# Performance work log

Measured on AMD Instinct MI355X. Metric: run time of the kernel, lower is better.

## Reference

```python
import jax, jax.numpy as jnp
import numpy as np

B, S, C, M, L = 32, 8192, 64, 16, 4  # batch, seq, n_enc, n_modes, n_layers


def setup_inputs() -> dict:
    key = jax.random.key(0)
    ks = jax.random.split(key, 12)
    scale = 1.0 / (C * M)
    return {
        "input_tensor": jax.random.normal(ks[0], (B, S, 1), dtype=jnp.float32),
        "enc_w": jax.random.normal(ks[1], (C, 1), dtype=jnp.float32) * 0.1,
        "enc_b": jax.random.normal(ks[2], (C,), dtype=jnp.float32) * 0.1,
        "R_re": jax.random.normal(ks[3], (L, C, C, M), dtype=jnp.float32) * scale,
        "R_im": jax.random.normal(ks[4], (L, C, C, M), dtype=jnp.float32) * scale,
        "Wl_w": jax.random.normal(ks[5], (L, C, C), dtype=jnp.float32) * 0.1,
        "Wl_b": jax.random.normal(ks[6], (L, C), dtype=jnp.float32) * 0.1,
        "d1_w": jax.random.normal(ks[7], (C, C), dtype=jnp.float32) * 0.1,
        "d1_b": jax.random.normal(ks[8], (C,), dtype=jnp.float32) * 0.1,
        "d2_w": jax.random.normal(ks[9], (1, C), dtype=jnp.float32) * 0.1,
        "d2_b": jax.random.normal(ks[10], (1,), dtype=jnp.float32) * 0.1,
    }


def reference(input_tensor, enc_w, enc_b, R_re, R_im, Wl_w, Wl_b, d1_w, d1_b, d2_w, d2_b):
    # encoder: Conv1d(1, C, k=1) == per-position dense over channel dim
    h = jnp.einsum('bsi,ci->bsc', input_tensor, enc_w) + enc_b  # [B,S,C]
    n_freq = S // 2 + 1
    for l in range(L):
        x_cs = jnp.swapaxes(h, 1, 2)                 # [B,C,S]
        x_ft = jnp.fft.rfft(x_cs, axis=-1)           # [B,C,n_freq] complex
        Rl = R_re[l] + 1j * R_im[l]                  # [C,C,M]
        y = jnp.einsum('bim,iom->bom', x_ft[:, :, :M], Rl)  # [B,C,M]
        y_full = jnp.concatenate(
            [y, jnp.zeros((B, C, n_freq - M), dtype=y.dtype)], axis=-1)
        spat = jnp.fft.irfft(y_full, n=S, axis=-1)   # [B,C,S] float32
        wout = jnp.einsum('oi,bis->bos', Wl_w[l], x_cs) + Wl_b[l][None, :, None]
        h = jax.nn.gelu(jnp.swapaxes(spat + wout, 1, 2), approximate=False)
    z = jax.nn.gelu(jnp.einsum('bsc,oc->bso', h, d1_w) + d1_b, approximate=False)
    out = jnp.einsum('bso,po->bsp', z, d2_w) + d2_b  # [B,S,1]
    return out
```

## Files before the change

kernel.cpp:

```cpp
#include <hip/hip_runtime.h>
#include <math.h>

#define NB 32
#define NS 8192
#define NC 64
#define NM 16
#define NL 4
#define NM2 32
#define NSBF 32
#define TPOS 128
#define PAD 65

typedef float f16v __attribute__((ext_vector_type(16)));

static __device__ __forceinline__ f16v zero16() {
    f16v v;
    #pragma unroll
    for (int j = 0; j < 16; ++j) v[j] = 0.0f;
    return v;
}

static __device__ __forceinline__ float gelu_exact(float v) {
    return 0.5f * v * (1.0f + erff(v * 0.7071067811865475f));
}

__global__ void k_table(float* __restrict__ T) {
    int s = blockIdx.x * blockDim.x + threadIdx.x;
    if (s >= NS) return;
    const float w = 6.283185307179586f / (float)NS;
    float* row = T + (size_t)s * NM2;
    #pragma unroll
    for (int m = 0; m < NM; ++m) {
        int idx = (m * s) & (NS - 1);
        float a = w * (float)idx;
        float sv, cv;
        sincosf(a, &sv, &cv);
        row[2*m]   = cv;
        row[2*m+1] = sv;
    }
}

__global__ void k_prep(const float* __restrict__ Ww, const float* __restrict__ d1w,
                       float* __restrict__ Wt, float* __restrict__ d1t) {
    int idx = blockIdx.x * 256 + threadIdx.x;
    if (idx < NL*NC*NC) {
        int l = idx / (NC*NC), r = idx % (NC*NC);
        int i = r / NC, o = r % NC;
        Wt[idx] = Ww[(size_t)l*NC*NC + (size_t)o*NC + i];
    } else if (idx < NL*NC*NC + NC*NC) {
        int r = idx - NL*NC*NC;
        int i = r / NC, o = r % NC;
        d1t[r] = d1w[(size_t)o*NC + i];
    }
}

__global__ void __launch_bounds__(256) k_enc(const float* __restrict__ x,
                                             const float* __restrict__ ew,
                                             const float* __restrict__ eb,
                                             float* __restrict__ h) {
    int t = threadIdx.x;
    int base = blockIdx.x * 64;
    float4* hout = (float4*)(h + (size_t)base * NC);
    #pragma unroll
    for (int j = 0; j < 4; ++j) {
        int idx = t + 256*j;
        int sl = idx >> 4, q = idx & 15;
        float xv = x[base + sl];
        float4 w4 = ((const float4*)ew)[q];
        float4 b4 = ((const float4*)eb)[q];
        hout[idx] = make_float4(fmaf(xv, w4.x, b4.x), fmaf(xv, w4.y, b4.y),
                                fmaf(xv, w4.z, b4.z), fmaf(xv, w4.w, b4.w));
    }
}

__global__ void __launch_bounds__(256) k_fwd(const float* __restrict__ h,
                                             const float* __restrict__ T,
                                             float* __restrict__ partial) {
    __shared__ float red[4 * NC * 33];
    int b = blockIdx.y, sb = blockIdx.x;
    int t = threadIdx.x;
    int w = t >> 6, lane = t & 63;
    const int PPW = NS / NSBF / 4;
    f16v A0 = zero16(), A1 = zero16();
    int s0 = sb * (NS / NSBF) + w * PPW;
    const float* hp = h + ((size_t)b*NS + s0)*NC + lane;
    #pragma unroll 2
    for (int it = 0; it < PPW; ++it) {
        float hv = hp[(size_t)it * NC];
        int su = __builtin_amdgcn_readfirstlane(s0 + it);
        const f16v* tr = (const f16v*)(T + (size_t)su * NM2);
        A0 += hv * tr[0];
        A1 += hv * tr[1];
    }
    float* rr = &red[(w*NC + lane) * 33];
    #pragma unroll
    for (int j = 0; j < 16; ++j) rr[j] = A0[j];
    #pragma unroll
    for (int j = 0; j < 16; ++j) rr[16 + j] = A1[j];
    __syncthreads();
    float* pout = partial + ((size_t)b*NSBF + sb) * (NC*NM2);
    #pragma unroll
    for (int e = 0; e < (NC*NM2)/256; ++e) {
        int idx = t + 256*e;
        int c = idx >> 5, k = idx & 31;
        pout[idx] = red[c*33 + k] + red[(NC + c)*33 + k]
                  + red[(2*NC + c)*33 + k] + red[(3*NC + c)*33 + k];
    }
}

__global__ void __launch_bounds__(256) k_mix(const float* __restrict__ partial,
                                             const float* __restrict__ Rre,
                                             const float* __restrict__ Rim,
                                             float* __restrict__ yst, int l) {
    __shared__ float xf[NC*NM2];
    int b = blockIdx.x, jg = blockIdx.y, t = threadIdx.x;
    #pragma unroll
    for (int e = 0; e < (NC*NM2)/256; ++e) {
        int idx = t + 256*e;
        float s = 0.f;
        #pragma unroll 8
        for (int sb = 0; sb < NSBF; ++sb)
            s += partial[((size_t)b*NSBF + sb)*(NC*NM2) + idx];
        xf[idx] = s;
    }
    __syncthreads();
    {
        int p = t + 256*jg;
        int o = p >> 4, m = p & 15;
        float yre = 0.f, yim = 0.f;
        #pragma unroll 8
        for (int i = 0; i < NC; ++i) {
            float xr = xf[i*NM2 + 2*m];
            float xs = xf[i*NM2 + 2*m + 1];
            size_t ridx = (((size_t)l*NC + i)*NC + o)*NM + m;
            float rr = Rre[ridx], ri = Rim[ridx];
            yre = fmaf(xr, rr, yre); yre = fmaf(xs, ri, yre);
            yim = fmaf(xr, ri, yim); yim = fmaf(-xs, rr, yim);
        }
        float* yb = yst + (size_t)b*NM2*NC;
        if (m == 0) { yb[o] = yre * (1.0f/NS); yb[NC + o] = 0.f; }
        else {
            yb[(size_t)(2*m)*NC + o]   = yre * (2.0f/NS);
            yb[(size_t)(2*m+1)*NC + o] = -yim * (2.0f/NS);
        }
    }
}

__global__ void __launch_bounds__(256) k_spec(float* __restrict__ h,
                                              const float* __restrict__ yst,
                                              const float* __restrict__ Wt,
                                              const float* __restrict__ Wb,
                                              int l) {
    __shared__ float hs[TPOS * PAD];
    int b = blockIdx.y;
    int t = threadIdx.x;
    int og = __builtin_amdgcn_readfirstlane(t >> 6);
    int p  = t & 63;
    int s0 = blockIdx.x * TPOS;

    const float4* hblk = (const float4*)(h + ((size_t)b*NS + s0)*NC);
    float4 ld0 = hblk[t];
    float4 ld1 = hblk[t + 256];
    float4 ld2 = hblk[t + 512];
    float4 ld3 = hblk[t + 768];
    float4 ld4 = hblk[t + 1024];
    float4 ld5 = hblk[t + 1280];
    float4 ld6 = hblk[t + 1536];
    float4 ld7 = hblk[t + 1792];

    const float* Wl = Wt + (size_t)l*NC*NC + og*16;
    const float* bl = Wb + (size_t)l*NC + og*16;
    const float* yb = yst + (size_t)b*NM2*NC + og*16;

    f16v accA = *(const f16v*)bl;
    f16v accB = accA;

    {
        f16v y0 = *(const f16v*)yb;
        accA += y0;
        accB += y0;
        const float w1 = 6.283185307179586f / (float)NS;
        float angA = (float)(s0 + p) * w1;
        float angB = (float)(s0 + p + 64) * w1;
        float cA1, sA1, cB1, sB1;
        sincosf(angA, &sA1, &cA1);
        sincosf(angB, &sB1, &cB1);
        float cmA = cA1, smA = sA1, cmB = cB1, smB = sB1;
        #pragma unroll 1
        for (int m = 1; m < NM; ++m) {
            f16v yc  = *(const f16v*)(yb + (size_t)(2*m)*NC);
            f16v ysv = *(const f16v*)(yb + (size_t)(2*m+1)*NC);
            accA += cmA * yc;  accA += smA * ysv;
            accB += cmB * yc;  accB += smB * ysv;
            float cnA = cmA*cA1 - smA*sA1;
            smA = cmA*sA1 + smA*cA1;  cmA = cnA;
            float cnB = cmB*cB1 - smB*sB1;
            smB = cmB*sB1 + smB*cB1;  cmB = cnB;
        }
    }

    {
        int ss = t >> 4, q4 = (t & 15) * 4;
        float* d;
        d = &hs[ss*PAD + q4];        d[0]=ld0.x; d[1]=ld0.y; d[2]=ld0.z; d[3]=ld0.w;
        d = &hs[(ss+16)*PAD + q4];   d[0]=ld1.x; d[1]=ld1.y; d[2]=ld1.z; d[3]=ld1.w;
        d = &hs[(ss+32)*PAD + q4];   d[0]=ld2.x; d[1]=ld2.y; d[2]=ld2.z; d[3]=ld2.w;
        d = &hs[(ss+48)*PAD + q4];   d[0]=ld3.x; d[1]=ld3.y; d[2]=ld3.z; d[3]=ld3.w;
        d = &hs[(ss+64)*PAD + q4];   d[0]=ld4.x; d[1]=ld4.y; d[2]=ld4.z; d[3]=ld4.w;
        d = &hs[(ss+80)*PAD + q4];   d[0]=ld5.x; d[1]=ld5.y; d[2]=ld5.z; d[3]=ld5.w;
        d = &hs[(ss+96)*PAD + q4];   d[0]=ld6.x; d[1]=ld6.y; d[2]=ld6.z; d[3]=ld6.w;
        d = &hs[(ss+112)*PAD + q4];  d[0]=ld7.x; d[1]=ld7.y; d[2]=ld7.z; d[3]=ld7.w;
    }
    __syncthreads();

    const float* hA = &hs[p * PAD];
    const float* hB = &hs[(p + 64) * PAD];
    #pragma unroll 8
    for (int i = 0; i < NC; ++i) {
        float va = hA[i], vb = hB[i];
        f16v w = *(const f16v*)(Wl + (size_t)i*NC);
        accA += va * w;
        accB += vb * w;
    }

    float* hpA = h + ((size_t)b*NS + s0 + p)*NC + og*16;
    float* hpB = h + ((size_t)b*NS + s0 + p + 64)*NC + og*16;
    f16v g;
    #pragma unroll
    for (int j = 0; j < 16; ++j) g[j] = gelu_exact(accA[j]);
    *(f16v*)hpA = g;
    #pragma unroll
    for (int j = 0; j < 16; ++j) g[j] = gelu_exact(accB[j]);
    *(f16v*)hpB = g;
}

__global__ void __launch_bounds__(256) k_dec(const float* __restrict__ h,
                                             const float* __restrict__ d1t,
                                             const float* __restrict__ d1b,
                                             const float* __restrict__ d2w,
                                             const float* __restrict__ d2b,
                                             float* __restrict__ out) {
    __shared__ float hs[TPOS * PAD];
    __shared__ float red[4 * TPOS];
    int t = threadIdx.x;
    int og = __builtin_amdgcn_readfirstlane(t >> 6);
    int p  = t & 63;
    int p0 = blockIdx.x * TPOS;

    const float4* hblk = (const float4*)(h + (size_t)p0 * NC);
    float4 ld0 = hblk[t];
    float4 ld1 = hblk[t + 256];
    float4 ld2 = hblk[t + 512];
    float4 ld3 = hblk[t + 768];
    float4 ld4 = hblk[t + 1024];
    float4 ld5 = hblk[t + 1280];
    float4 ld6 = hblk[t + 1536];
    float4 ld7 = hblk[t + 1792];
    {
        int ss = t >> 4, q4 = (t & 15) * 4;
        float* d;
        d = &hs[ss*PAD + q4];        d[0]=ld0.x; d[1]=ld0.y; d[2]=ld0.z; d[3]=ld0.w;
        d = &hs[(ss+16)*PAD + q4];   d[0]=ld1.x; d[1]=ld1.y; d[2]=ld1.z; d[3]=ld1.w;
        d = &hs[(ss+32)*PAD + q4];   d[0]=ld2.x; d[1]=ld2.y; d[2]=ld2.z; d[3]=ld2.w;
        d = &hs[(ss+48)*PAD + q4];   d[0]=ld3.x; d[1]=ld3.y; d[2]=ld3.z; d[3]=ld3.w;
        d = &hs[(ss+64)*PAD + q4];   d[0]=ld4.x; d[1]=ld4.y; d[2]=ld4.z; d[3]=ld4.w;
        d = &hs[(ss+80)*PAD + q4];   d[0]=ld5.x; d[1]=ld5.y; d[2]=ld5.z; d[3]=ld5.w;
        d = &hs[(ss+96)*PAD + q4];   d[0]=ld6.x; d[1]=ld6.y; d[2]=ld6.z; d[3]=ld6.w;
        d = &hs[(ss+112)*PAD + q4];  d[0]=ld7.x; d[1]=ld7.y; d[2]=ld7.z; d[3]=ld7.w;
    }
    __syncthreads();

    f16v accA = *(const f16v*)(d1b + og*16);
    f16v accB = accA;
    const float* hA = &hs[p * PAD];
    const float* hB = &hs[(p + 64) * PAD];
    #pragma unroll 8
    for (int i = 0; i < NC; ++i) {
        float va = hA[i], vb = hB[i];
        f16v w = *(const f16v*)(d1t + (size_t)i*NC + og*16);
        accA += va * w;
        accB += vb * w;
    }
    float resA = 0.f, resB = 0.f;
    #pragma unroll
    for (int j = 0; j < 16; ++j) {
        float dw = d2w[og*16 + j];
        resA = fmaf(gelu_exact(accA[j]), dw, resA);
        resB = fmaf(gelu_exact(accB[j]), dw, resB);
    }
    red[og*TPOS + p]      = resA;
    red[og*TPOS + p + 64] = resB;
    __syncthreads();
    if (t < TPOS) {
        out[p0 + t] = d2b[0] + red[t] + red[TPOS + t]
                    + red[2*TPOS + t] + red[3*TPOS + t];
    }
}

extern "C" void kernel_launch(void* const* d_in, const int* in_sizes, int n_in,
                              void* d_out, int out_size, void* d_ws, size_t ws_size,
                              hipStream_t stream) {
    const float* input = (const float*)d_in[0];
    const float* enc_w = (const float*)d_in[1];
    const float* enc_b = (const float*)d_in[2];
    const float* R_re  = (const float*)d_in[3];
    const float* R_im  = (const float*)d_in[4];
    const float* Wl_w  = (const float*)d_in[5];
    const float* Wl_b  = (const float*)d_in[6];
    const float* d1_w  = (const float*)d_in[7];
    const float* d1_b  = (const float*)d_in[8];
    const float* d2_w  = (const float*)d_in[9];
    const float* d2_b  = (const float*)d_in[10];
    float* out = (float*)d_out;

    float* ws  = (float*)d_ws;
    float* h   = ws;
    float* T   = h   + (size_t)NB*NS*NC;
    float* par = T   + (size_t)NS*NM2;
    float* yst = par + (size_t)NB*NSBF*NC*NM2;
    float* Wt  = yst + (size_t)NB*NM2*NC;
    float* d1t = Wt  + (size_t)NL*NC*NC;

    hipLaunchKernelGGL(k_table, dim3(NS/256), dim3(256), 0, stream, T);
    hipLaunchKernelGGL(k_prep, dim3((NL*NC*NC + NC*NC + 255)/256), dim3(256), 0,
                       stream, Wl_w, d1_w, Wt, d1t);
    hipLaunchKernelGGL(k_enc, dim3((NB*NS)/64), dim3(256), 0, stream,
                       input, enc_w, enc_b, h);
    for (int l = 0; l < NL; ++l) {
        hipLaunchKernelGGL(k_fwd, dim3(NSBF, NB), dim3(256), 0, stream, h, T, par);
        hipLaunchKernelGGL(k_mix, dim3(NB, 4), dim3(256), 0, stream,
                           par, R_re, R_im, yst, l);
        hipLaunchKernelGGL(k_spec, dim3(NS/TPOS, NB), dim3(256), 0, stream,
                           h, yst, Wt, Wl_b, l);
    }
    hipLaunchKernelGGL(k_dec, dim3((NB*NS)/TPOS), dim3(256), 0, stream,
                       h, d1t, d1_b, d2_w, d2_b, out);
}
```

Measured before the change: 402.7 us.

## Fuse forward DFT projection into encoder and spectral layer kernels, fold decoder into last layer

Moves the truncated-DFT projection onto the first 16 modes into the epilogue of the encoder and spectral-layer kernels. It works on the tile already in shared memory, so the separate k_fwd pass that re-read h from global memory is gone. The last layer computes the decoder MLP in place and never writes h back, which removes the k_dec kernel and one full read and write of h. The cost is more partial sums (64 tiles per batch instead of 32) for k_mix to reduce, extra shared-memory syncs, and more register pressure in the spectral kernel.

```diff
diff --git a/kernel.cpp b/kernel.cpp
--- a/kernel.cpp
+++ b/kernel.cpp
@@ -7,16 +7,17 @@
 #define NM 16
 #define NL 4
 #define NM2 32
-#define NSBF 32
 #define TPOS 128
+#define NT (NS/TPOS)
 #define PAD 65
 
 typedef float f16v __attribute__((ext_vector_type(16)));
-
-static __device__ __forceinline__ f16v zero16() {
-    f16v v;
-    #pragma unroll
-    for (int j = 0; j < 16; ++j) v[j] = 0.0f;
+typedef float f8v  __attribute__((ext_vector_type(8)));
+
+static __device__ __forceinline__ f8v zero8() {
+    f8v v;
+    #pragma unroll
+    for (int j = 0; j < 8; ++j) v[j] = 0.0f;
     return v;
 }
 
@@ -54,84 +55,81 @@
     }
 }
 
+static __device__ __forceinline__ void dft_phase(
+        const float* __restrict__ hs, const float* __restrict__ T,
+        float* __restrict__ partial, int b, int tile, int s0,
+        int og, int t) {
+    int c = t & 63;
+    f8v acc = zero8();
+    const float* trow = T + (size_t)s0 * NM2 + og * 8;
+    #pragma unroll 4
+    for (int ss = 0; ss < TPOS; ++ss) {
+        float hv = hs[ss * PAD + c];
+        f8v tv = *(const f8v*)(trow + (size_t)ss * NM2);
+        acc += hv * tv;
+    }
+    float* pout = partial + (((size_t)b*NT + tile)*NC + c)*NM2 + og*8;
+    *(f8v*)pout = acc;
+}
+
 __global__ void __launch_bounds__(256) k_enc(const float* __restrict__ x,
                                              const float* __restrict__ ew,
                                              const float* __restrict__ eb,
-                                             float* __restrict__ h) {
+                                             const float* __restrict__ T,
+                                             float* __restrict__ h,
+                                             float* __restrict__ partial) {
+    __shared__ float hs[TPOS * PAD];
+    int tile = blockIdx.x, b = blockIdx.y;
     int t = threadIdx.x;
-    int base = blockIdx.x * 64;
-    float4* hout = (float4*)(h + (size_t)base * NC);
-    #pragma unroll
-    for (int j = 0; j < 4; ++j) {
-        int idx = t + 256*j;
-        int sl = idx >> 4, q = idx & 15;
-        float xv = x[base + sl];
-        float4 w4 = ((const float4*)ew)[q];
-        float4 b4 = ((const float4*)eb)[q];
-        hout[idx] = make_float4(fmaf(xv, w4.x, b4.x), fmaf(xv, w4.y, b4.y),
-                                fmaf(xv, w4.z, b4.z), fmaf(xv, w4.w, b4.w));
-    }
-}
-
-__global__ void __launch_bounds__(256) k_fwd(const float* __restrict__ h,
-                                             const float* __restrict__ T,
-                                             float* __restrict__ partial) {
-    __shared__ float red[4 * NC * 33];
-    int b = blockIdx.y, sb = blockIdx.x;
-    int t = threadIdx.x;
-    int w = t >> 6, lane = t & 63;
-    const int PPW = NS / NSBF / 4;
-    f16v A0 = zero16(), A1 = zero16();
-    int s0 = sb * (NS / NSBF) + w * PPW;
-    const float* hp = h + ((size_t)b*NS + s0)*NC + lane;
-    #pragma unroll 2
-    for (int it = 0; it < PPW; ++it) {
-        float hv = hp[(size_t)it * NC];
-        int su = __builtin_amdgcn_readfirstlane(s0 + it);
-        const f16v* tr = (const f16v*)(T + (size_t)su * NM2);
-        A0 += hv * tr[0];
-        A1 += hv * tr[1];
-    }
-    float* rr = &red[(w*NC + lane) * 33];
-    #pragma unroll
-    for (int j = 0; j < 16; ++j) rr[j] = A0[j];
-    #pragma unroll
-    for (int j = 0; j < 16; ++j) rr[16 + j] = A1[j];
-    __syncthreads();
-    float* pout = partial + ((size_t)b*NSBF + sb) * (NC*NM2);
-    #pragma unroll
-    for (int e = 0; e < (NC*NM2)/256; ++e) {
-        int idx = t + 256*e;
-        int c = idx >> 5, k = idx & 31;
-        pout[idx] = red[c*33 + k] + red[(NC + c)*33 + k]
-                  + red[(2*NC + c)*33 + k] + red[(3*NC + c)*33 + k];
-    }
+    int og = __builtin_amdgcn_readfirstlane(t >> 6);
+    int p  = t & 63;
+    int s0 = tile * TPOS;
+
+    float xA = x[(size_t)b*NS + s0 + p];
+    float xB = x[(size_t)b*NS + s0 + p + 64];
+    f16v ew16 = *(const f16v*)(ew + og*16);
+    f16v eb16 = *(const f16v*)(eb + og*16);
+    f16v hA = xA * ew16 + eb16;
+    f16v hB = xB * ew16 + eb16;
+
+    *(f16v*)(h + ((size_t)b*NS + s0 + p)*NC + og*16)      = hA;
+    *(f16v*)(h + ((size_t)b*NS + s0 + p + 64)*NC + og*16) = hB;
+
+    #pragma unroll
+    for (int j = 0; j < 16; ++j) hs[p*PAD + og*16 + j] = hA[j];
+    #pragma unroll
+    for (int j = 0; j < 16; ++j) hs[(p+64)*PAD + og*16 + j] = hB[j];
+    __syncthreads();
+
+    dft_phase(hs, T, partial, b, tile, s0, og, t);
 }
 
 __global__ void __launch_bounds__(256) k_mix(const float* __restrict__ partial,
                                              const float* __restrict__ Rre,
                                              const float* __restrict__ Rim,
                                              float* __restrict__ yst, int l) {
-    __shared__ float xf[NC*NM2];
+    __shared__ float xf[NC * 8];
     int b = blockIdx.x, jg = blockIdx.y, t = threadIdx.x;
     #pragma unroll
-    for (int e = 0; e < (NC*NM2)/256; ++e) {
+    for (int e = 0; e < 2; ++e) {
         int idx = t + 256*e;
+        int c = idx >> 3, kk = idx & 7;
+        const float* pp = partial + (size_t)b*NT*NC*NM2 + (size_t)c*NM2 + 8*jg + kk;
         float s = 0.f;
         #pragma unroll 8
-        for (int sb = 0; sb < NSBF; ++sb)
-            s += partial[((size_t)b*NSBF + sb)*(NC*NM2) + idx];
+        for (int tile = 0; tile < NT; ++tile)
+            s += pp[(size_t)tile * NC * NM2];
         xf[idx] = s;
     }
     __syncthreads();
     {
-        int p = t + 256*jg;
-        int o = p >> 4, m = p & 15;
+        int o = t >> 2, mq = t & 3;
+        int m = 4*jg + mq;
         float yre = 0.f, yim = 0.f;
         #pragma unroll 8
         for (int i = 0; i < NC; ++i) {
-            float xr = xf[i*NM2 + 2*m];
-            float xs = xf[i*NM2 + 2*m + 1];
+            float xr = xf[i*8 + 2*mq];
+            float xs = xf[i*8 + 2*mq + 1];
             size_t ridx = (((size_t)l*NC + i)*NC + o)*NM + m;
             float rr = Rre[ridx], ri = Rim[ridx];
             yre = fmaf(xr, rr, yre); yre = fmaf(xs, ri, yre);
@@ -146,17 +144,26 @@
     }
 }
 
+template<bool LAST>
 __global__ void __launch_bounds__(256) k_spec(float* __restrict__ h,
+                                              const float* __restrict__ T,
                                               const float* __restrict__ yst,
                                               const float* __restrict__ Wt,
                                               const float* __restrict__ Wb,
+                                              const float* __restrict__ d1t,
+                                              const float* __restrict__ d1b,
+                                              const float* __restrict__ d2w,
+                                              const float* __restrict__ d2b,
+                                              float* __restrict__ partial,
+                                              float* __restrict__ outp,
                                               int l) {
     __shared__ float hs[TPOS * PAD];
-    int b = blockIdx.y;
+    __shared__ float red[4 * TPOS];
+    int tile = blockIdx.x, b = blockIdx.y;
     int t = threadIdx.x;
     int og = __builtin_amdgcn_readfirstlane(t >> 6);
     int p  = t & 63;
-    int s0 = blockIdx.x * TPOS;
+    int s0 = tile * TPOS;
 
     const float4* hblk = (const float4*)(h + ((size_t)b*NS + s0)*NC);
     float4 ld0 = hblk[t];
@@ -223,77 +230,49 @@
         accB += vb * w;
     }
 
-    float* hpA = h + ((size_t)b*NS + s0 + p)*NC + og*16;
-    float* hpB = h + ((size_t)b*NS + s0 + p + 64)*NC + og*16;
-    f16v g;
-    #pragma unroll
-    for (int j = 0; j < 16; ++j) g[j] = gelu_exact(accA[j]);
-    *(f16v*)hpA = g;
-    #pragma unroll
-    for (int j = 0; j < 16; ++j) g[j] = gelu_exact(accB[j]);
-    *(f16v*)hpB = g;
-}
-
-__global__ void __launch_bounds__(256) k_dec(const float* __restrict__ h,
-                                             const float* __restrict__ d1t,
-                                             const float* __restrict__ d1b,
-                                             const float* __restrict__ d2w,
-                                             const float* __restrict__ d2b,
-                                             float* __restrict__ out) {
-    __shared__ float hs[TPOS * PAD];
-    __shared__ float red[4 * TPOS];
-    int t = threadIdx.x;
-    int og = __builtin_amdgcn_readfirstlane(t >> 6);
-    int p  = t & 63;
-    int p0 = blockIdx.x * TPOS;
-
-    const float4* hblk = (const float4*)(h + (size_t)p0 * NC);
-    float4 ld0 = hblk[t];
-    float4 ld1 = hblk[t + 256];
-    float4 ld2 = hblk[t + 512];
-    float4 ld3 = hblk[t + 768];
-    float4 ld4 = hblk[t + 1024];
-    float4 ld5 = hblk[t + 1280];
-    float4 ld6 = hblk[t + 1536];
-    float4 ld7 = hblk[t + 1792];
-    {
-        int ss = t >> 4, q4 = (t & 15) * 4;
-        float* d;
-        d = &hs[ss*PAD + q4];        d[0]=ld0.x; d[1]=ld0.y; d[2]=ld0.z; d[3]=ld0.w;
-        d = &hs[(ss+16)*PAD + q4];   d[0]=ld1.x; d[1]=ld1.y; d[2]=ld1.z; d[3]=ld1.w;
-        d = &hs[(ss+32)*PAD + q4];   d[0]=ld2.x; d[1]=ld2.y; d[2]=ld2.z; d[3]=ld2.w;
-        d = &hs[(ss+48)*PAD + q4];   d[0]=ld3.x; d[1]=ld3.y; d[2]=ld3.z; d[3]=ld3.w;
-        d = &hs[(ss+64)*PAD + q4];   d[0]=ld4.x; d[1]=ld4.y; d[2]=ld4.z; d[3]=ld4.w;
-        d = &hs[(ss+80)*PAD + q4];   d[0]=ld5.x; d[1]=ld5.y; d[2]=ld5.z; d[3]=ld5.w;
-        d = &hs[(ss+96)*PAD + q4];   d[0]=ld6.x; d[1]=ld6.y; d[2]=ld6.z; d[3]=ld6.w;
-        d = &hs[(ss+112)*PAD + q4];  d[0]=ld7.x; d[1]=ld7.y; d[2]=ld7.z; d[3]=ld7.w;
-    }
-    __syncthreads();
-
-    f16v accA = *(const f16v*)(d1b + og*16);
-    f16v accB = accA;
-    const float* hA = &hs[p * PAD];
-    const float* hB = &hs[(p + 64) * PAD];
-    #pragma unroll 8
-    for (int i = 0; i < NC; ++i) {
-        float va = hA[i], vb = hB[i];
-        f16v w = *(const f16v*)(d1t + (size_t)i*NC + og*16);
-        accA += va * w;
-        accB += vb * w;
-    }
-    float resA = 0.f, resB = 0.f;
-    #pragma unroll
-    for (int j = 0; j < 16; ++j) {
-        float dw = d2w[og*16 + j];
-        resA = fmaf(gelu_exact(accA[j]), dw, resA);
-        resB = fmaf(gelu_exact(accB[j]), dw, resB);
-    }
-    red[og*TPOS + p]      = resA;
-    red[og*TPOS + p + 64] = resB;
-    __syncthreads();
-    if (t < TPOS) {
-        out[p0 + t] = d2b[0] + red[t] + red[TPOS + t]
-                    + red[2*TPOS + t] + red[3*TPOS + t];
+    f16v gA, gB;
+    #pragma unroll
+    for (int j = 0; j < 16; ++j) gA[j] = gelu_exact(accA[j]);
+    #pragma unroll
+    for (int j = 0; j < 16; ++j) gB[j] = gelu_exact(accB[j]);
+    if (!LAST) {
+        *(f16v*)(h + ((size_t)b*NS + s0 + p)*NC + og*16)      = gA;
+        *(f16v*)(h + ((size_t)b*NS + s0 + p + 64)*NC + og*16) = gB;
+    }
+
+    __syncthreads();
+    #pragma unroll
+    for (int j = 0; j < 16; ++j) hs[p*PAD + og*16 + j] = gA[j];
+    #pragma unroll
+    for (int j = 0; j < 16; ++j) hs[(p+64)*PAD + og*16 + j] = gB[j];
+    __syncthreads();
+
+    if (!LAST) {
+        dft_phase(hs, T, partial, b, tile, s0, og, t);
+    } else {
+        f16v aA = *(const f16v*)(d1b + og*16);
+        f16v aB = aA;
+        #pragma unroll 8
+        for (int i = 0; i < NC; ++i) {
+            float va = hA[i], vb = hB[i];
+            f16v w = *(const f16v*)(d1t + (size_t)i*NC + og*16);
+            aA += va * w;
+            aB += vb * w;
+        }
+        float resA = 0.f, resB = 0.f;
+        #pragma unroll
+        for (int j = 0; j < 16; ++j) {
+            float dw = d2w[og*16 + j];
+            resA = fmaf(gelu_exact(aA[j]), dw, resA);
+            resB = fmaf(gelu_exact(aB[j]), dw, resB);
+        }
+        red[og*TPOS + p]      = resA;
+        red[og*TPOS + p + 64] = resB;
+        __syncthreads();
+        if (t < TPOS) {
+            outp[(size_t)b*NS + s0 + t] = d2b[0] + red[t] + red[TPOS + t]
+                                        + red[2*TPOS + t] + red[3*TPOS + t];
+        }
     }
 }
 
@@ -317,22 +296,26 @@
     float* h   = ws;
     float* T   = h   + (size_t)NB*NS*NC;
     float* par = T   + (size_t)NS*NM2;
-    float* yst = par + (size_t)NB*NSBF*NC*NM2;
+    float* yst = par + (size_t)NB*NT*NC*NM2;
     float* Wt  = yst + (size_t)NB*NM2*NC;
     float* d1t = Wt  + (size_t)NL*NC*NC;
 
     hipLaunchKernelGGL(k_table, dim3(NS/256), dim3(256), 0, stream, T);
     hipLaunchKernelGGL(k_prep, dim3((NL*NC*NC + NC*NC + 255)/256), dim3(256), 0,
                        stream, Wl_w, d1_w, Wt, d1t);
-    hipLaunchKernelGGL(k_enc, dim3((NB*NS)/64), dim3(256), 0, stream,
-                       input, enc_w, enc_b, h);
+    hipLaunchKernelGGL(k_enc, dim3(NT, NB), dim3(256), 0, stream,
+                       input, enc_w, enc_b, T, h, par);
     for (int l = 0; l < NL; ++l) {
-        hipLaunchKernelGGL(k_fwd, dim3(NSBF, NB), dim3(256), 0, stream, h, T, par);
         hipLaunchKernelGGL(k_mix, dim3(NB, 4), dim3(256), 0, stream,
                            par, R_re, R_im, yst, l);
-        hipLaunchKernelGGL(k_spec, dim3(NS/TPOS, NB), dim3(256), 0, stream,
-                           h, yst, Wt, Wl_b, l);
-    }
-    hipLaunchKernelGGL(k_dec, dim3((NB*NS)/TPOS), dim3(256), 0, stream,
-                       h, d1t, d1_b, d2_w, d2_b, out);
-}
+        if (l < NL - 1) {
+            hipLaunchKernelGGL((k_spec<false>), dim3(NT, NB), dim3(256), 0, stream,
+                               h, T, yst, Wt, Wl_b, d1t, d1_b, d2_w, d2_b,
+                               par, out, l);
+        } else {
+            hipLaunchKernelGGL((k_spec<true>), dim3(NT, NB), dim3(256), 0, stream,
+                               h, T, yst, Wt, Wl_b, d1t, d1_b, d2_w, d2_b,
+                               par, out, l);
+        }
+    }
+}
```

Measured after the change: 363.3 us. 1.11x faster.
